# Kernel optimization log

Hardware: AMD Instinct MI355X
Metric: run time of the kernel (lower is better)

## Reference

```python
import jax, jax.numpy as jnp
import numpy as np

H = 256  # hidden_size
T = 4096  # sequence length
IN = 128  # input_size


def _lstm_dir(x_seq, Wih, Whh, b, reverse):
    # x_seq: [T, D_in]; Wih: [4H, D_in]; Whh: [4H, H]; b: [4H]
    xs = x_seq @ Wih.T + b  # precompute input projection [T, 4H]
    if reverse:
        xs = xs[::-1]

    def step(carry, xt):
        h, c = carry
        z = xt + h @ Whh.T
        i, f, g, o = jnp.split(z, 4, axis=-1)  # torch gate order i,f,g,o
        c = jax.nn.sigmoid(f) * c + jax.nn.sigmoid(i) * jnp.tanh(g)
        h = jax.nn.sigmoid(o) * jnp.tanh(c)
        return (h, c), h

    init = (jnp.zeros((H,), x_seq.dtype), jnp.zeros((H,), x_seq.dtype))
    _, hs = jax.lax.scan(step, init, xs)
    if reverse:
        hs = hs[::-1]
    return hs  # [T, H]


def _bilstm_layer(x_seq, Wih_f, Whh_f, b_f, Wih_b, Whh_b, b_b):
    hf = _lstm_dir(x_seq, Wih_f, Whh_f, b_f, False)
    hb = _lstm_dir(x_seq, Wih_b, Whh_b, b_b, True)
    return jnp.concatenate([hf, hb], axis=-1)  # [T, 2H]


def setup_inputs() -> dict:
    key = jax.random.key(0)
    ks = jax.random.split(key, 20)
    s = 1.0 / np.sqrt(H)

    def g(k, shape):
        return (jax.random.normal(k, shape, dtype=jnp.float32) * s)

    inp = {
        "x": jax.random.normal(ks[0], (1, T, IN), dtype=jnp.float32),
        # layer 0 (input dim IN), fwd / bwd directions; b = b_ih + b_hh folded
        "wih_l0f": g(ks[1], (4 * H, IN)), "whh_l0f": g(ks[2], (4 * H, H)), "b_l0f": g(ks[3], (4 * H,)),
        "wih_l0b": g(ks[4], (4 * H, IN)), "whh_l0b": g(ks[5], (4 * H, H)), "b_l0b": g(ks[6], (4 * H,)),
        # layer 1 (input dim 2H)
        "wih_l1f": g(ks[7], (4 * H, 2 * H)), "whh_l1f": g(ks[8], (4 * H, H)), "b_l1f": g(ks[9], (4 * H,)),
        "wih_l1b": g(ks[10], (4 * H, 2 * H)), "whh_l1b": g(ks[11], (4 * H, H)), "b_l1b": g(ks[12], (4 * H,)),
        # fc1: Linear(512, 256); fc2: Linear(256, 256)
        "fc1_w": g(ks[13], (256, 512)), "fc1_b": g(ks[14], (256,)),
        "fc2_w": g(ks[15], (256, 256)), "fc2_b": g(ks[16], (256,)),
    }
    return inp


def reference(x, wih_l0f, whh_l0f, b_l0f, wih_l0b, whh_l0b, b_l0b,
              wih_l1f, whh_l1f, b_l1f, wih_l1b, whh_l1b, b_l1b,
              fc1_w, fc1_b, fc2_w, fc2_b):
    xs = x[0]  # squeeze batch of 1 -> [T, IN]
    h1 = _bilstm_layer(xs, wih_l0f, whh_l0f, b_l0f, wih_l0b, whh_l0b, b_l0b)  # [T, 512]
    h2 = _bilstm_layer(h1, wih_l1f, whh_l1f, b_l1f, wih_l1b, whh_l1b, b_l1b)  # [T, 512]
    z = jnp.maximum(h2 @ fc1_w.T + fc1_b, 0.0)  # ReLU(fc1)
    e = z @ fc2_w.T + fc2_b  # [T, 256]
    # fused pairwise cosine similarity (replaces the per-row python loop)
    norms = jnp.linalg.norm(e, axis=1)  # [T]
    cs = (e @ e.T) / (norms[:, None] * norms[None, :])
    cs = jnp.maximum(cs, 1e-6)  # torch.clamp(min=1e-6)
    return 1.0 - cs  # [T, T]
```

## Files before the change

kernel.cpp:

```cpp
#include <hip/hip_runtime.h>
#include <hip/hip_fp16.h>

#define T_LEN 4096
#define HID   256
#define G4    1024

typedef unsigned int u32;
typedef _Float16 half2_t __attribute__((ext_vector_type(2)));

__device__ __forceinline__ float dot2f(u32 w, u32 h, float acc) {
#if __has_builtin(__builtin_amdgcn_fdot2)
    return __builtin_amdgcn_fdot2(__builtin_bit_cast(half2_t, w),
                                  __builtin_bit_cast(half2_t, h), acc, false);
#else
    __half2 wh = __builtin_bit_cast(__half2, w);
    __half2 hh = __builtin_bit_cast(__half2, h);
    float2 wf = __half22float2(wh), hf = __half22float2(hh);
    return acc + wf.x * hf.x + wf.y * hf.y;
#endif
}

__device__ __forceinline__ u32 pack2(float a, float b) {
    unsigned short lo = __half_as_ushort(__float2half(a));
    unsigned short hi = __half_as_ushort(__float2half(b));
    return ((u32)hi << 16) | (u32)lo;
}

__global__ void k_transpose(const float* __restrict__ in, float* __restrict__ out,
                            int N, int K) {
    int q = blockIdx.x * 256 + threadIdx.x;
    if (q >= N * K) return;
    int n = q / K, k = q % K;
    out[(size_t)k * N + n] = in[q];
}

__global__ void k_pack_whh(const float* __restrict__ W,
                           u32* __restrict__ rp, u32* __restrict__ lp) {
    int q = blockIdx.x * 256 + threadIdx.x;
    if (q < 512 * 192) {
        int tid = q / 192, j = q % 192;
        int row = (j < 96) ? tid : tid + 512;
        int p = j % 96;
        rp[q] = pack2(W[row * 256 + 2 * p], W[row * 256 + 2 * p + 1]);
    } else {
        int qq = q - 512 * 192;
        if (qq < 1024 * 32) {
            int row = qq / 32, j = qq % 32;
            lp[qq] = pack2(W[row * 256 + 192 + 2 * j], W[row * 256 + 192 + 2 * j + 1]);
        }
    }
}

__global__ __launch_bounds__(256) void k_gemm(
    const float* __restrict__ A, const float* __restrict__ Wt,
    const float* __restrict__ bias, const float* __restrict__ norms,
    float* __restrict__ C, int M, int N, int K, int mode) {
    __shared__ float As[16 * 512];
    const int tid = threadIdx.x;
    const int m0 = blockIdx.x * 16;
    const int n  = blockIdx.y * 256 + tid;

    for (int i = tid; i < 16 * K; i += 256) As[i] = A[(size_t)m0 * K + i];
    __syncthreads();

    float acc[16];
#pragma unroll
    for (int m = 0; m < 16; ++m) acc[m] = 0.f;

#pragma unroll 4
    for (int k = 0; k < K; ++k) {
        float w = Wt[(size_t)k * N + n];
#pragma unroll
        for (int m = 0; m < 16; ++m) acc[m] += As[m * K + k] * w;
    }

    float bn = bias ? bias[n] : 0.f;
#pragma unroll
    for (int m = 0; m < 16; ++m) {
        float v = acc[m] + bn;
        if (mode == 1) v = fmaxf(v, 0.f);
        if (mode == 2) {
            float d = norms[m0 + m] * norms[n];
            v = 1.f - fmaxf(acc[m] / d, 1e-6f);
        }
        C[(size_t)(m0 + m) * N + n] = v;
    }
}

__global__ void k_norms(const float* __restrict__ e, float* __restrict__ norms) {
    int i = blockIdx.x, lane = threadIdx.x;
    float s = 0.f;
    for (int k = lane; k < 256; k += 64) { float v = e[i * 256 + k]; s += v * v; }
    for (int off = 32; off; off >>= 1) s += __shfl_down(s, off);
    if (lane == 0) norms[i] = sqrtf(s);
}

__global__ __launch_bounds__(512, 2) void k_scan(
    const float* __restrict__ xs, const u32* __restrict__ rp,
    const u32* __restrict__ lp, float* __restrict__ hout) {
    __shared__ alignas(16) u32 wl[1024 * 34];
    __shared__ alignas(16) u32 hlds[128];
    __shared__ float zsh[512];

    const int tid = threadIdx.x;
    const int dir = blockIdx.x;
    xs += (size_t)dir * (T_LEN * G4);
    rp += (size_t)dir * (512 * 192);
    lp += (size_t)dir * (1024 * 32);

    for (int i = tid; i < 1024 * 32; i += 512) {
        int row = i >> 5, j = i & 31;
        wl[row * 34 + j] = lp[i];
    }
    if (tid < 128) hlds[tid] = 0u;

    u32 regw[192];
    {
        const uint4* rp4 = (const uint4*)(rp + (size_t)tid * 192);
#pragma unroll
        for (int p = 0; p < 48; ++p) {
            uint4 v = rp4[p];
            regw[4 * p + 0] = v.x; regw[4 * p + 1] = v.y;
            regw[4 * p + 2] = v.z; regw[4 * p + 3] = v.w;
        }
    }
    const int r0 = tid, r1 = tid + 512;
    float cst = 0.f;
    __syncthreads();

    int tt = dir ? (T_LEN - 1) : 0;
    float xn0 = xs[(size_t)tt * G4 + r0];
    float xn1 = xs[(size_t)tt * G4 + r1];

    for (int t = 0; t < T_LEN; ++t) {
        float a0 = xn0, a1 = xn1;
        int tn = dir ? ((t + 1 < T_LEN) ? T_LEN - 2 - t : 0)
                     : ((t + 1 < T_LEN) ? t + 1 : T_LEN - 1);
        xn0 = xs[(size_t)tn * G4 + r0];
        xn1 = xs[(size_t)tn * G4 + r1];

#pragma unroll
        for (int c = 0; c < 3; ++c) {
            u32 hh[32];
#pragma unroll
            for (int q = 0; q < 8; ++q) {
                uint4 v = *(const uint4*)&hlds[c * 32 + 4 * q];
                hh[4 * q + 0] = v.x; hh[4 * q + 1] = v.y;
                hh[4 * q + 2] = v.z; hh[4 * q + 3] = v.w;
            }
#pragma unroll
            for (int p = 0; p < 32; ++p) {
                a0 = dot2f(regw[c * 32 + p],      hh[p], a0);
                a1 = dot2f(regw[96 + c * 32 + p], hh[p], a1);
            }
        }
#pragma unroll
        for (int s = 0; s < 4; ++s) {
            u32 hh[8], w0[8], w1[8];
            uint4 hv0 = *(const uint4*)&hlds[96 + 8 * s];
            uint4 hv1 = *(const uint4*)&hlds[96 + 8 * s + 4];
            hh[0] = hv0.x; hh[1] = hv0.y; hh[2] = hv0.z; hh[3] = hv0.w;
            hh[4] = hv1.x; hh[5] = hv1.y; hh[6] = hv1.z; hh[7] = hv1.w;
#pragma unroll
            for (int u = 0; u < 4; ++u) {
                uint2 wa = *(const uint2*)&wl[r0 * 34 + 8 * s + 2 * u];
                w0[2 * u] = wa.x; w0[2 * u + 1] = wa.y;
                uint2 wb = *(const uint2*)&wl[r1 * 34 + 8 * s + 2 * u];
                w1[2 * u] = wb.x; w1[2 * u + 1] = wb.y;
            }
#pragma unroll
            for (int p = 0; p < 8; ++p) {
                a0 = dot2f(w0[p], hh[p], a0);
                a1 = dot2f(w1[p], hh[p], a1);
            }
        }

        if (tid >= 256) { zsh[tid - 256] = a0; zsh[256 + (tid - 256)] = a1; }
        __syncthreads();
        if (tid < 256) {
            float zi = a0, zg = a1;
            float zf = zsh[tid], zo = zsh[256 + tid];
            float si = 1.f / (1.f + __expf(-zi));
            float sf = 1.f / (1.f + __expf(-zf));
            float so = 1.f / (1.f + __expf(-zo));
            float tg = 1.f - 2.f / (__expf(2.f * zg) + 1.f);
            cst = sf * cst + si * tg;
            float th = 1.f - 2.f / (__expf(2.f * cst) + 1.f);
            float hv = so * th;
            hout[(size_t)tt * 512 + dir * 256 + tid] = hv;
            ((__half*)hlds)[tid] = __float2half(hv);
        }
        __syncthreads();
        tt = tn;
    }
}

extern "C" void kernel_launch(void* const* d_in, const int* in_sizes, int n_in,
                              void* d_out, int out_size, void* d_ws, size_t ws_size,
                              hipStream_t stream) {
    const float* x       = (const float*)d_in[0];
    const float* wih_l0f = (const float*)d_in[1];
    const float* whh_l0f = (const float*)d_in[2];
    const float* b_l0f   = (const float*)d_in[3];
    const float* wih_l0b = (const float*)d_in[4];
    const float* whh_l0b = (const float*)d_in[5];
    const float* b_l0b   = (const float*)d_in[6];
    const float* wih_l1f = (const float*)d_in[7];
    const float* whh_l1f = (const float*)d_in[8];
    const float* b_l1f   = (const float*)d_in[9];
    const float* wih_l1b = (const float*)d_in[10];
    const float* whh_l1b = (const float*)d_in[11];
    const float* b_l1b   = (const float*)d_in[12];
    const float* fc1_w   = (const float*)d_in[13];
    const float* fc1_b   = (const float*)d_in[14];
    const float* fc2_w   = (const float*)d_in[15];
    const float* fc2_b   = (const float*)d_in[16];
    float* outp = (float*)d_out;

    char* ws = (char*)d_ws;
    size_t off = 0;
    auto alloc = [&](size_t nbytes) {
        char* p = ws + off;
        off += (nbytes + 255) & ~(size_t)255;
        return p;
    };
    float* xs0   = (float*)alloc((size_t)2 * T_LEN * G4 * 4);
    float* xs1   = (float*)alloc((size_t)2 * T_LEN * G4 * 4);
    float* h1    = (float*)alloc((size_t)T_LEN * 512 * 4);
    float* h2    = (float*)alloc((size_t)T_LEN * 512 * 4);
    float* zb    = (float*)alloc((size_t)T_LEN * 256 * 4);
    float* eb    = (float*)alloc((size_t)T_LEN * 256 * 4);
    float* etb   = (float*)alloc((size_t)T_LEN * 256 * 4);
    float* nrm   = (float*)alloc((size_t)T_LEN * 4);
    float* wt0f  = (float*)alloc((size_t)128 * 1024 * 4);
    float* wt0b  = (float*)alloc((size_t)128 * 1024 * 4);
    float* wt1f  = (float*)alloc((size_t)512 * 1024 * 4);
    float* wt1b  = (float*)alloc((size_t)512 * 1024 * 4);
    float* wtf1  = (float*)alloc((size_t)512 * 256 * 4);
    float* wtf2  = (float*)alloc((size_t)256 * 256 * 4);
    u32*   rp0   = (u32*)alloc((size_t)2 * 512 * 192 * 4);
    u32*   lp0   = (u32*)alloc((size_t)2 * 1024 * 32 * 4);
    u32*   rp1   = (u32*)alloc((size_t)2 * 512 * 192 * 4);
    u32*   lp1   = (u32*)alloc((size_t)2 * 1024 * 32 * 4);

    k_transpose<<<(1024 * 128 + 255) / 256, 256, 0, stream>>>(wih_l0f, wt0f, 1024, 128);
    k_transpose<<<(1024 * 128 + 255) / 256, 256, 0, stream>>>(wih_l0b, wt0b, 1024, 128);
    k_transpose<<<(1024 * 512 + 255) / 256, 256, 0, stream>>>(wih_l1f, wt1f, 1024, 512);
    k_transpose<<<(1024 * 512 + 255) / 256, 256, 0, stream>>>(wih_l1b, wt1b, 1024, 512);
    k_transpose<<<(256 * 512 + 255) / 256, 256, 0, stream>>>(fc1_w, wtf1, 256, 512);
    k_transpose<<<(256 * 256 + 255) / 256, 256, 0, stream>>>(fc2_w, wtf2, 256, 256);

    const int packN = (512 * 192 + 1024 * 32 + 255) / 256;
    k_pack_whh<<<packN, 256, 0, stream>>>(whh_l0f, rp0,                lp0);
    k_pack_whh<<<packN, 256, 0, stream>>>(whh_l0b, rp0 + 512 * 192,    lp0 + 1024 * 32);
    k_pack_whh<<<packN, 256, 0, stream>>>(whh_l1f, rp1,                lp1);
    k_pack_whh<<<packN, 256, 0, stream>>>(whh_l1b, rp1 + 512 * 192,    lp1 + 1024 * 32);

    dim3 g1024(T_LEN / 16, 4);
    k_gemm<<<g1024, 256, 0, stream>>>(x, wt0f, b_l0f, nullptr, xs0, T_LEN, 1024, 128, 0);
    k_gemm<<<g1024, 256, 0, stream>>>(x, wt0b, b_l0b, nullptr, xs0 + (size_t)T_LEN * G4, T_LEN, 1024, 128, 0);
    k_scan<<<2, 512, 0, stream>>>(xs0, rp0, lp0, h1);
    k_gemm<<<g1024, 256, 0, stream>>>(h1, wt1f, b_l1f, nullptr, xs1, T_LEN, 1024, 512, 0);
    k_gemm<<<g1024, 256, 0, stream>>>(h1, wt1b, b_l1b, nullptr, xs1 + (size_t)T_LEN * G4, T_LEN, 1024, 512, 0);
    k_scan<<<2, 512, 0, stream>>>(xs1, rp1, lp1, h2);
    k_gemm<<<dim3(T_LEN / 16, 1), 256, 0, stream>>>(h2, wtf1, fc1_b, nullptr, zb, T_LEN, 256, 512, 1);
    k_gemm<<<dim3(T_LEN / 16, 1), 256, 0, stream>>>(zb, wtf2, fc2_b, nullptr, eb, T_LEN, 256, 256, 0);
    k_transpose<<<(T_LEN * 256 + 255) / 256, 256, 0, stream>>>(eb, etb, T_LEN, 256);
    k_norms<<<T_LEN, 64, 0, stream>>>(eb, nrm);
    k_gemm<<<dim3(T_LEN / 16, T_LEN / 256), 256, 0, stream>>>(eb, etb, nullptr, nrm, outp, T_LEN, T_LEN, 256, 2);
}
```

Measured before the change: 14.81 ms.

## Pair gate rows across adjacent lanes and double-buffer h to drop one barrier

Threads are remapped so each adjacent lane pair holds all four gate rows (i,g and f,o) of one hidden unit. The gates are exchanged with xor shuffles instead of going through shared memory, and both lanes compute the cell update redundantly. The hidden state is double-buffered in LDS, so each timestep needs only one custom barrier instead of two __syncthreads. The cost is duplicated activation math on every lane and a barrier that relies on hand-placed s_waitcnt and sched_barrier ordering.

Result: slower. 18.89 ms (+27.5%).

```diff
diff --git a/kernel.cpp b/kernel.cpp
--- a/kernel.cpp
+++ b/kernel.cpp
@@ -26,6 +26,12 @@
     return ((u32)hi << 16) | (u32)lo;
 }
 
+__device__ __forceinline__ void step_barrier() {
+    asm volatile("s_waitcnt lgkmcnt(0)" ::: "memory");
+    __builtin_amdgcn_s_barrier();
+    __builtin_amdgcn_sched_barrier(0);
+}
+
 __global__ void k_transpose(const float* __restrict__ in, float* __restrict__ out,
                             int N, int K) {
     int q = blockIdx.x * 256 + threadIdx.x;
@@ -39,7 +45,9 @@
     int q = blockIdx.x * 256 + threadIdx.x;
     if (q < 512 * 192) {
         int tid = q / 192, j = q % 192;
-        int row = (j < 96) ? tid : tid + 512;
+        int mm = tid >> 1, pr = tid & 1;
+        int rbase = mm + pr * 256;
+        int row = (j < 96) ? rbase : rbase + 512;
         int p = j % 96;
         rp[q] = pack2(W[row * 256 + 2 * p], W[row * 256 + 2 * p + 1]);
     } else {
@@ -99,11 +107,12 @@
     const float* __restrict__ xs, const u32* __restrict__ rp,
     const u32* __restrict__ lp, float* __restrict__ hout) {
     __shared__ alignas(16) u32 wl[1024 * 34];
-    __shared__ alignas(16) u32 hlds[128];
-    __shared__ float zsh[512];
+    __shared__ alignas(16) u32 hb[2][128];
 
     const int tid = threadIdx.x;
     const int dir = blockIdx.x;
+    const int m   = tid >> 1;
+    const int par = tid & 1;
     xs += (size_t)dir * (T_LEN * G4);
     rp += (size_t)dir * (512 * 192);
     lp += (size_t)dir * (1024 * 32);
@@ -112,7 +121,7 @@
         int row = i >> 5, j = i & 31;
         wl[row * 34 + j] = lp[i];
     }
-    if (tid < 128) hlds[tid] = 0u;
+    if (tid < 128) { hb[0][tid] = 0u; hb[1][tid] = 0u; }
 
     u32 regw[192];
     {
@@ -124,7 +133,8 @@
             regw[4 * p + 2] = v.z; regw[4 * p + 3] = v.w;
         }
     }
-    const int r0 = tid, r1 = tid + 512;
+    const int r0 = m + par * 256;
+    const int r1 = r0 + 512;
     float cst = 0.f;
     __syncthreads();
 
@@ -139,12 +149,14 @@
         xn0 = xs[(size_t)tn * G4 + r0];
         xn1 = xs[(size_t)tn * G4 + r1];
 
+        const u32* rd = hb[t & 1];
+
 #pragma unroll
         for (int c = 0; c < 3; ++c) {
             u32 hh[32];
 #pragma unroll
             for (int q = 0; q < 8; ++q) {
-                uint4 v = *(const uint4*)&hlds[c * 32 + 4 * q];
+                uint4 v = *(const uint4*)&rd[c * 32 + 4 * q];
                 hh[4 * q + 0] = v.x; hh[4 * q + 1] = v.y;
                 hh[4 * q + 2] = v.z; hh[4 * q + 3] = v.w;
             }
@@ -156,41 +168,44 @@
         }
 #pragma unroll
         for (int s = 0; s < 4; ++s) {
-            u32 hh[8], w0[8], w1[8];
-            uint4 hv0 = *(const uint4*)&hlds[96 + 8 * s];
-            uint4 hv1 = *(const uint4*)&hlds[96 + 8 * s + 4];
+            u32 hh[8];
+            uint4 hv0 = *(const uint4*)&rd[96 + 8 * s];
+            uint4 hv1 = *(const uint4*)&rd[96 + 8 * s + 4];
             hh[0] = hv0.x; hh[1] = hv0.y; hh[2] = hv0.z; hh[3] = hv0.w;
             hh[4] = hv1.x; hh[5] = hv1.y; hh[6] = hv1.z; hh[7] = hv1.w;
 #pragma unroll
             for (int u = 0; u < 4; ++u) {
                 uint2 wa = *(const uint2*)&wl[r0 * 34 + 8 * s + 2 * u];
-                w0[2 * u] = wa.x; w0[2 * u + 1] = wa.y;
                 uint2 wb = *(const uint2*)&wl[r1 * 34 + 8 * s + 2 * u];
-                w1[2 * u] = wb.x; w1[2 * u + 1] = wb.y;
+                a0 = dot2f(wa.x, hh[2 * u],     a0);
+                a0 = dot2f(wa.y, hh[2 * u + 1], a0);
+                a1 = dot2f(wb.x, hh[2 * u],     a1);
+                a1 = dot2f(wb.y, hh[2 * u + 1], a1);
             }
-#pragma unroll
-            for (int p = 0; p < 8; ++p) {
-                a0 = dot2f(w0[p], hh[p], a0);
-                a1 = dot2f(w1[p], hh[p], a1);
-            }
-        }
-
-        if (tid >= 256) { zsh[tid - 256] = a0; zsh[256 + (tid - 256)] = a1; }
-        __syncthreads();
-        if (tid < 256) {
-            float zi = a0, zg = a1;
-            float zf = zsh[tid], zo = zsh[256 + tid];
-            float si = 1.f / (1.f + __expf(-zi));
-            float sf = 1.f / (1.f + __expf(-zf));
-            float so = 1.f / (1.f + __expf(-zo));
-            float tg = 1.f - 2.f / (__expf(2.f * zg) + 1.f);
-            cst = sf * cst + si * tg;
-            float th = 1.f - 2.f / (__expf(2.f * cst) + 1.f);
-            float hv = so * th;
-            hout[(size_t)tt * 512 + dir * 256 + tid] = hv;
-            ((__half*)hlds)[tid] = __float2half(hv);
-        }
-        __syncthreads();
+        }
+
+        float s0 = __shfl_xor(a0, 1);
+        float s1 = __shfl_xor(a1, 1);
+        float zi = par ? s0 : a0;
+        float zf = par ? a0 : s0;
+        float zg = par ? s1 : a1;
+        float zo = par ? a1 : s1;
+
+        float si = 1.f / (1.f + __expf(-zi));
+        float sf = 1.f / (1.f + __expf(-zf));
+        float so = 1.f / (1.f + __expf(-zo));
+        float tg = 1.f - 2.f / (__expf(2.f * zg) + 1.f);
+        cst = sf * cst + si * tg;
+        float th = 1.f - 2.f / (__expf(2.f * cst) + 1.f);
+        float hv = so * th;
+
+        u32* wr = (u32*)hb[(t & 1) ^ 1];
+        if (par) {
+            hout[(size_t)tt * 512 + dir * 256 + m] = hv;
+        } else {
+            ((__half*)wr)[m] = __float2half(hv);
+        }
+        step_barrier();
         tt = tn;
     }
 }
```
